# Kernel tuning notes

Hardware: AMD Instinct MI355X
Metric: run time of the kernel (lower is better)

The kernel has to match this reference:

```python
import jax, jax.numpy as jnp
import numpy as np

IN_FEATURES = 128
DEPTH = 2
UNITS = 512
BATCH = 2048
W_SCALE = 0.02


def _create_masks():
    degrees = [np.arange(IN_FEATURES)]
    for _ in range(DEPTH):
        degrees.append(np.arange(UNITS) % (IN_FEATURES - 1))
    degrees.append(degrees[0] % IN_FEATURES - 1)
    masks = []
    for d1, d2 in zip(degrees[:-1], degrees[1:]):
        masks.append(np.greater_equal(d2[:, None], d1[None, :]).astype('float32'))
    masks[-1] = np.tile(masks[-1], (2, 1))  # final layer outputs [mu; sigma]
    return masks


def setup_inputs() -> dict:
    key = jax.random.key(0)
    ks = jax.random.split(key, 7)
    m1, m2, m3 = _create_masks()
    u = jax.random.normal(ks[0], (BATCH, IN_FEATURES), dtype=jnp.float32)
    # torch.nn.Linear weight layout: [out_features, in_features]
    W1 = jax.random.normal(ks[1], (UNITS, IN_FEATURES), dtype=jnp.float32) * W_SCALE
    b1 = jax.random.normal(ks[2], (UNITS,), dtype=jnp.float32) * W_SCALE
    W2 = jax.random.normal(ks[3], (UNITS, UNITS), dtype=jnp.float32) * W_SCALE
    b2 = jax.random.normal(ks[4], (UNITS,), dtype=jnp.float32) * W_SCALE
    W3 = jax.random.normal(ks[5], (2 * IN_FEATURES, UNITS), dtype=jnp.float32) * W_SCALE
    b3 = jax.random.normal(ks[6], (2 * IN_FEATURES,), dtype=jnp.float32) * W_SCALE
    return {
        'u': u,
        'W1': W1, 'b1': b1, 'W2': W2, 'b2': b2, 'W3': W3, 'b3': b3,
        'mask1': jnp.asarray(m1), 'mask2': jnp.asarray(m2), 'mask3': jnp.asarray(m3),
    }


def reference(u, W1, b1, W2, b2, W3, b3, mask1, mask2, mask3):
    # Pre-apply masks once; math identical to masking inside every step.
    mW1 = mask1 * W1
    mW2 = mask2 * W2
    mW3 = mask3 * W3

    def conditioner(x):
        h = jax.nn.relu(x @ mW1.T + b1)
        h = jax.nn.relu(h @ mW2.T + b2)
        z = h @ mW3.T + b3  # [B, 2*IN_FEATURES]
        return z[:, :IN_FEATURES], z[:, IN_FEATURES:]  # mu, sigma

    def step(x, i):
        mu, sigma = conditioner(x)
        mu_i = jnp.take(mu, i, axis=1)        # [B]
        sig_i = jnp.take(sigma, i, axis=1)    # [B]
        u_i = jnp.take(u, i, axis=1)          # [B]
        x = x.at[:, i].set(u_i * jnp.exp(sig_i) + mu_i)
        return x, sig_i

    x0 = jnp.zeros_like(u)
    x, sigs = jax.lax.scan(step, x0, jnp.arange(IN_FEATURES))
    # sigs: [IN_FEATURES, B]; log_det_jacobian = sum_i sigma_i -> [B, 1]
    log_det_jacobian = jnp.sum(sigs, axis=0)[:, None]
    return x, log_det_jacobian
```

## Files before the change

kernel.cpp:

```cpp
#include <hip/hip_runtime.h>
#include <math.h>

static constexpr int BATCH = 2048;
static constexpr int P1_OFF = 0;
static constexpr int P2_OFF = 128 * 512;
static constexpr int P3_OFF = 128 * 512 + 512 * 512;


__device__ __forceinline__ float fc(float4 v, int k) {
    return k == 0 ? v.x : k == 1 ? v.y : k == 2 ? v.z : v.w;
}
__device__ __forceinline__ float rl(float v, int l) {
    return __int_as_float(__builtin_amdgcn_readlane(__float_as_int(v), l));
}

__global__ __launch_bounds__(256) void maf_prep(
    const float* __restrict__ W1, const float* __restrict__ W2,
    const float* __restrict__ W3, float* __restrict__ ws)
{
    float* P1 = ws + P1_OFF;
    float* P2 = ws + P2_OFF;
    float* P3 = ws + P3_OFF;
    const int NQ1 = 512 * 128 / 4;
    const int NQ2 = 512 * 512 / 4;
    const int NQ3 = 256 * 512 / 4;
    for (int q = blockIdx.x * blockDim.x + threadIdx.x; q < NQ1 + NQ2 + NQ3;
         q += gridDim.x * blockDim.x) {
        if (q < NQ1) {
            int j = q >> 5, i0 = (q & 31) * 4;
            float4 v = *(const float4*)(W1 + j * 128 + i0);
            int dj = j % 127;
            int sj = (j < 508) ? 4 * dj + (j / 127) : j;
#pragma unroll
            for (int c = 0; c < 4; ++c) {
                int i = i0 + c;
                P1[i * 512 + sj] = (dj >= i) ? fc(v, c) : 0.f;
            }
        } else if (q < NQ1 + NQ2) {
            int e = q - NQ1;
            int k = e >> 7, j0 = (e & 127) * 4;
            float4 v = *(const float4*)(W2 + k * 512 + j0);
            int dk = k % 127;
            int sk = (k < 508) ? 4 * dk + (k / 127) : k;
#pragma unroll
            for (int c = 0; c < 4; ++c) {
                int j = j0 + c;
                int dj = j % 127;
                int sj = (j < 508) ? 4 * dj + (j / 127) : j;
                P2[sj * 512 + sk] = (dk >= dj) ? fc(v, c) : 0.f;
            }
        } else {
            int e = q - NQ1 - NQ2;
            int o = e >> 7, k0 = (e & 127) * 4;
            float4 v = *(const float4*)(W3 + o * 512 + k0);
            int dd = (o & 127) - 1;
#pragma unroll
            for (int c = 0; c < 4; ++c) {
                int k = k0 + c;
                int dk = k % 127;
                int sk = (k < 508) ? 4 * dk + (k / 127) : k;
                P3[sk * 256 + o] = (dd >= dk) ? fc(v, c) : 0.f;
            }
        }
    }
}

#define DECL_WSET(P) \
    float4 P##0{}, P##1{}, P##2{}, P##3{}, P##4{}, P##5{}, P##6{}, P##7{}, \
           P##8{}, P##9{}, P##10{}, P##11{}, P##12{}, P##13{};

#define LOADS(P, LO) do { \
    if (LO) { \
        P##0 = *(const float4*)(q1); \
        P##2 = *(const float4*)(q2a); \
        P##4 = *(const float4*)(q2a + 512); \
        P##6 = *(const float4*)(q2b); \
        P##8 = *(const float4*)(q2b + 512); \
    } \
    P##1  = *(const float4*)(q1 + 256); \
    P##3  = *(const float4*)(q2a + 256); \
    P##5  = *(const float4*)(q2a + 768); \
    P##7  = *(const float4*)(q2b + 256); \
    P##9  = *(const float4*)(q2b + 768); \
    P##10 = *(const float4*)(q3); \
    P##11 = *(const float4*)(q3 + 256); \
    P##12 = *(const float4*)(q3 + 512); \
    P##13 = *(const float4*)(q3 + 768); \
    q1 += 512; q2a += 2048; q2b += 2048; q3 += 1024; \
    __builtin_amdgcn_sched_barrier(0); \
} while (0)

#define L2T(T, WLO, WHI, LO) do { \
    const float hA = rl(fmaxf(LO ? h1A[T] : h1A[4 + (T)], 0.f), l0); \
    const float hB = rl(fmaxf(LO ? h1B[T] : h1B[4 + (T)], 0.f), l0); \
    if (LO) { \
        _Pragma("unroll") for (int r = 0; r < 4; ++r) { \
            h2A[r] = fmaf(fc(WLO, r), hA, h2A[r]); \
            h2B[r] = fmaf(fc(WLO, r), hB, h2B[r]); } \
    } \
    _Pragma("unroll") for (int r = 0; r < 4; ++r) { \
        h2A[4 + r] = fmaf(fc(WHI, r), hA, h2A[4 + r]); \
        h2B[4 + r] = fmaf(fc(WHI, r), hB, h2B[4 + r]); } \
} while (0)

#define L3T(T, W4, LO) do { \
    const float gA = rl(fmaxf(LO ? h2A[T] : h2A[4 + (T)], 0.f), l0); \
    const float gB = rl(fmaxf(LO ? h2B[T] : h2B[4 + (T)], 0.f), l0); \
    _Pragma("unroll") for (int s = 0; s < 4; ++s) { \
        zA[s] = fmaf(fc(W4, s), gA, zA[s]); \
        zB[s] = fmaf(fc(W4, s), gB, zB[s]); } \
} while (0)

#define STEP(I, P, LO) do { \
    const int l0 = (I) & 63, lm = (I) >> 2, rs = (I) & 3; \
    float zsA = rs == 0 ? zA[0] : rs == 1 ? zA[1] : rs == 2 ? zA[2] : zA[3]; \
    float zsB = rs == 0 ? zB[0] : rs == 1 ? zB[1] : rs == 2 ? zB[2] : zB[3]; \
    const float muA = rl(zsA, lm), sgA = rl(zsA, 32 + lm); \
    const float muB = rl(zsB, lm), sgB = rl(zsB, 32 + lm); \
    const float uiA = rl(LO ? uA0 : uA1, l0); \
    const float uiB = rl(LO ? uB0 : uB1, l0); \
    const float xiA = fmaf(uiA, __expf(sgA), muA); \
    const float xiB = fmaf(uiB, __expf(sgB), muB); \
    ldA += sgA; ldB += sgB; \
    if (lane == l0) { \
        if (LO) { xA0 = xiA; xB0 = xiB; } else { xA1 = xiA; xB1 = xiB; } \
    } \
    if (LO) { \
        _Pragma("unroll") for (int r = 0; r < 4; ++r) { \
            h1A[r] = fmaf(fc(P##0, r), xiA, h1A[r]); \
            h1B[r] = fmaf(fc(P##0, r), xiB, h1B[r]); } \
    } \
    _Pragma("unroll") for (int r = 0; r < 4; ++r) { \
        h1A[4 + r] = fmaf(fc(P##1, r), xiA, h1A[4 + r]); \
        h1B[4 + r] = fmaf(fc(P##1, r), xiB, h1B[4 + r]); } \
    L2T(0, P##2, P##3, LO); \
    L2T(1, P##4, P##5, LO); \
    L2T(2, P##6, P##7, LO); \
    L2T(3, P##8, P##9, LO); \
    if (LO && (I) < 4) { \
        float eA = (I) == 0 ? h1A[4] : (I) == 1 ? h1A[5] : (I) == 2 ? h1A[6] : h1A[7]; \
        float eB = (I) == 0 ? h1B[4] : (I) == 1 ? h1B[5] : (I) == 2 ? h1B[6] : h1B[7]; \
        const float hA = rl(fmaxf(eA, 0.f), 63); \
        const float hB = rl(fmaxf(eB, 0.f), 63); \
        const float* wr = P2 + (508 + (I)) * 512 + 4 * lane; \
        const float4 wl = *(const float4*)(wr); \
        const float4 wh = *(const float4*)(wr + 256); \
        _Pragma("unroll") for (int r = 0; r < 4; ++r) { \
            h2A[r] = fmaf(fc(wl, r), hA, h2A[r]); \
            h2B[r] = fmaf(fc(wl, r), hB, h2B[r]); \
            h2A[4 + r] = fmaf(fc(wh, r), hA, h2A[4 + r]); \
            h2B[4 + r] = fmaf(fc(wh, r), hB, h2B[4 + r]); } \
    } \
    L3T(0, P##10, LO); \
    L3T(1, P##11, LO); \
    L3T(2, P##12, LO); \
    L3T(3, P##13, LO); \
    if (LO && (I) < 4) { \
        float eA = (I) == 0 ? h2A[4] : (I) == 1 ? h2A[5] : (I) == 2 ? h2A[6] : h2A[7]; \
        float eB = (I) == 0 ? h2B[4] : (I) == 1 ? h2B[5] : (I) == 2 ? h2B[6] : h2B[7]; \
        const float gA = rl(fmaxf(eA, 0.f), 63); \
        const float gB = rl(fmaxf(eB, 0.f), 63); \
        const float4 w4 = *(const float4*)(P3 + (508 + (I)) * 256 + 4 * lane); \
        _Pragma("unroll") for (int s = 0; s < 4; ++s) { \
            zA[s] = fmaf(fc(w4, s), gA, zA[s]); \
            zB[s] = fmaf(fc(w4, s), gB, zB[s]); } \
    } \
} while (0)

__global__ __launch_bounds__(256, 1) void maf_inverse(
    const float* __restrict__ u, const float* __restrict__ b1,
    const float* __restrict__ b2, const float* __restrict__ b3,
    const float* __restrict__ ws, float* __restrict__ out)
{
    const float* P1 = ws + P1_OFF;
    const float* P2 = ws + P2_OFF;
    const float* P3 = ws + P3_OFF;

    const int td = threadIdx.x;
    const int lane = td & 63;
    const int wid = td >> 6;
    const int rA = blockIdx.x * 8 + wid * 2;
    const int rB = rA + 1;

    float h1A[8], h1B[8], h2A[8], h2B[8];
#pragma unroll
    for (int r = 0; r < 8; ++r) {
        int s = (r < 4) ? (4 * lane + r) : (256 + 4 * lane + (r - 4));
        int i = s >> 2, t = s & 3;
        int uu = (i == 127) ? (508 + t) : (127 * t + i);
        float v1 = b1[uu], v2 = b2[uu];
        h1A[r] = v1; h1B[r] = v1; h2A[r] = v2; h2B[r] = v2;
    }
    float zA[4], zB[4];
    {
        const float4 bz = *(const float4*)(b3 + 4 * lane);
        zA[0] = bz.x; zA[1] = bz.y; zA[2] = bz.z; zA[3] = bz.w;
        zB[0] = bz.x; zB[1] = bz.y; zB[2] = bz.z; zB[3] = bz.w;
    }
    const float uA0 = u[rA * 128 + lane], uA1 = u[rA * 128 + 64 + lane];
    const float uB0 = u[rB * 128 + lane], uB1 = u[rB * 128 + 64 + lane];

    float xA0 = 0.f, xA1 = 0.f, xB0 = 0.f, xB1 = 0.f, ldA = 0.f, ldB = 0.f;

    const float* q1  = P1 + 4 * lane;
    const float* q2a = P2 + 4 * lane;
    const float* q2b = P2 + 1024 + 4 * lane;
    const float* q3  = P3 + 4 * lane;

    DECL_WSET(wa)
    DECL_WSET(wb)

    LOADS(wa, true);
#pragma unroll 1
    for (int i = 0; i < 62; i += 2) {
        LOADS(wb, true);
        STEP(i, wa, true);
        LOADS(wa, true);
        STEP(i + 1, wb, true);
    }
    LOADS(wb, true);
    STEP(62, wa, true);
    LOADS(wa, false);
    STEP(63, wb, true);
#pragma unroll 1
    for (int i = 64; i < 126; i += 2) {
        LOADS(wb, false);
        STEP(i, wa, false);
        LOADS(wa, false);
        STEP(i + 1, wb, false);
    }
    STEP(126, wa, false);

    {
        const float muA = rl(zA[3], 31), sgA = rl(zA[3], 63);
        const float muB = rl(zB[3], 31), sgB = rl(zB[3], 63);
        const float uiA = rl(uA1, 63), uiB = rl(uB1, 63);
        const float xiA = fmaf(uiA, __expf(sgA), muA);
        const float xiB = fmaf(uiB, __expf(sgB), muB);
        ldA += sgA; ldB += sgB;
        if (lane == 63) { xA1 = xiA; xB1 = xiB; }
    }

    out[rA * 128 + lane]      = xA0;
    out[rA * 128 + 64 + lane] = xA1;
    out[rB * 128 + lane]      = xB0;
    out[rB * 128 + 64 + lane] = xB1;
    if (lane == 0) {
        out[BATCH * 128 + rA] = ldA;
        out[BATCH * 128 + rB] = ldB;
    }
}

extern "C" void kernel_launch(void* const* d_in, const int* in_sizes, int n_in,
                              void* d_out, int out_size, void* d_ws, size_t ws_size,
                              hipStream_t stream)
{
    const float* u  = (const float*)d_in[0];
    const float* W1 = (const float*)d_in[1];
    const float* b1 = (const float*)d_in[2];
    const float* W2 = (const float*)d_in[3];
    const float* b2 = (const float*)d_in[4];
    const float* W3 = (const float*)d_in[5];
    const float* b3 = (const float*)d_in[6];
    float* ws  = (float*)d_ws;
    float* out = (float*)d_out;
    (void)ws_size; (void)in_sizes; (void)n_in; (void)out_size;

    maf_prep<<<448, 256, 0, stream>>>(W1, W2, W3, ws);
    maf_inverse<<<256, 256, 0, stream>>>(u, b1, b2, b3, ws, out);
}
```

Baseline: 139.1 us.

## Transpose weights through LDS in prep and skip loads of masked-zero weight rows

The prep kernel now transposes and permutes each weight matrix through padded shared-memory tiles, so global reads and float4 writes are coalesced. It replaces the old scattered scalar stores and runs on 80 blocks instead of 448. In the main inverse kernel, each step's weight loads are predicated per lane on the autoregressive degree, so lanes whose weights are known zero skip the global loads and keep the zero-initialised registers. This reduces memory traffic but adds lane divergence and relies on the register sets being zero-initialised and never refilled.

```diff
diff --git a/kernel.cpp b/kernel.cpp
--- a/kernel.cpp
+++ b/kernel.cpp
@@ -6,6 +6,16 @@
 static constexpr int P2_OFF = 128 * 512;
 static constexpr int P3_OFF = 128 * 512 + 512 * 512;
 
+__device__ __forceinline__ int sigmaF(int x) {
+    return (x < 508) ? 4 * (x % 127) + (x / 127) : x;
+}
+__device__ __forceinline__ int sigmaInv(int s) {
+    int i = s >> 2, t = s & 3;
+    return (i == 127) ? (508 + t) : (127 * t + i);
+}
+__device__ __forceinline__ int degU(int x) {
+    return (x < 508) ? (x % 127) : (x - 508);
+}
 
 __device__ __forceinline__ float fc(float4 v, int k) {
     return k == 0 ? v.x : k == 1 ? v.y : k == 2 ? v.z : v.w;
@@ -18,49 +28,80 @@
     const float* __restrict__ W1, const float* __restrict__ W2,
     const float* __restrict__ W3, float* __restrict__ ws)
 {
-    float* P1 = ws + P1_OFF;
-    float* P2 = ws + P2_OFF;
-    float* P3 = ws + P3_OFF;
-    const int NQ1 = 512 * 128 / 4;
-    const int NQ2 = 512 * 512 / 4;
-    const int NQ3 = 256 * 512 / 4;
-    for (int q = blockIdx.x * blockDim.x + threadIdx.x; q < NQ1 + NQ2 + NQ3;
-         q += gridDim.x * blockDim.x) {
-        if (q < NQ1) {
-            int j = q >> 5, i0 = (q & 31) * 4;
-            float4 v = *(const float4*)(W1 + j * 128 + i0);
-            int dj = j % 127;
-            int sj = (j < 508) ? 4 * dj + (j / 127) : j;
-#pragma unroll
-            for (int c = 0; c < 4; ++c) {
-                int i = i0 + c;
-                P1[i * 512 + sj] = (dj >= i) ? fc(v, c) : 0.f;
-            }
-        } else if (q < NQ1 + NQ2) {
-            int e = q - NQ1;
-            int k = e >> 7, j0 = (e & 127) * 4;
+    __shared__ float lds[16 * 513];
+    const int td = threadIdx.x;
+    const int b = blockIdx.x;
+    if (b < 32) {
+        for (int e = 0; e < 8; ++e) {
+            int g = e * 256 + td;
+            int l = g >> 7, j0 = (g & 127) * 4;
+            int k = sigmaInv(16 * b + l);
+            int dk = degU(k);
             float4 v = *(const float4*)(W2 + k * 512 + j0);
-            int dk = k % 127;
-            int sk = (k < 508) ? 4 * dk + (k / 127) : k;
 #pragma unroll
             for (int c = 0; c < 4; ++c) {
                 int j = j0 + c;
-                int dj = j % 127;
-                int sj = (j < 508) ? 4 * dj + (j / 127) : j;
-                P2[sj * 512 + sk] = (dk >= dj) ? fc(v, c) : 0.f;
+                lds[l * 513 + sigmaF(j)] = (dk >= degU(j)) ? fc(v, c) : 0.f;
             }
-        } else {
-            int e = q - NQ1 - NQ2;
-            int o = e >> 7, k0 = (e & 127) * 4;
+        }
+        __syncthreads();
+        for (int e = 0; e < 8; ++e) {
+            int g = e * 256 + td;
+            int sj = g >> 2, c4 = g & 3;
+            float4 o4;
+            o4.x = lds[(4 * c4 + 0) * 513 + sj];
+            o4.y = lds[(4 * c4 + 1) * 513 + sj];
+            o4.z = lds[(4 * c4 + 2) * 513 + sj];
+            o4.w = lds[(4 * c4 + 3) * 513 + sj];
+            *(float4*)(ws + P2_OFF + sj * 512 + 16 * b + 4 * c4) = o4;
+        }
+    } else if (b < 64) {
+        int bb = b - 32;
+        for (int e = 0; e < 4; ++e) {
+            int g = e * 256 + td;
+            int ol = g >> 7, k0 = (g & 127) * 4;
+            int o = 8 * bb + ol;
+            int dd = (o & 127) - 1;
             float4 v = *(const float4*)(W3 + o * 512 + k0);
-            int dd = (o & 127) - 1;
 #pragma unroll
             for (int c = 0; c < 4; ++c) {
                 int k = k0 + c;
-                int dk = k % 127;
-                int sk = (k < 508) ? 4 * dk + (k / 127) : k;
-                P3[sk * 256 + o] = (dd >= dk) ? fc(v, c) : 0.f;
+                lds[sigmaF(k) * 9 + ol] = (dd >= degU(k)) ? fc(v, c) : 0.f;
             }
+        }
+        __syncthreads();
+        for (int e = 0; e < 4; ++e) {
+            int g = e * 256 + td;
+            int sk = g >> 1, h = (g & 1) * 4;
+            float4 o4;
+            o4.x = lds[sk * 9 + h + 0];
+            o4.y = lds[sk * 9 + h + 1];
+            o4.z = lds[sk * 9 + h + 2];
+            o4.w = lds[sk * 9 + h + 3];
+            *(float4*)(ws + P3_OFF + sk * 256 + 8 * bb + h) = o4;
+        }
+    } else {
+        int bb = b - 64;
+        for (int e = 0; e < 4; ++e) {
+            int g = e * 256 + td;
+            int l = g >> 5, i0 = (g & 31) * 4;
+            int j = sigmaInv(32 * bb + l);
+            int dj = degU(j);
+            float4 v = *(const float4*)(W1 + j * 128 + i0);
+#pragma unroll
+            for (int c = 0; c < 4; ++c)
+                lds[l * 129 + i0 + c] = (dj >= i0 + c) ? fc(v, c) : 0.f;
+        }
+        __syncthreads();
+        for (int e = 0; e < 4; ++e) {
+            int g = e * 256 + td;
+            int i = g >> 3, c4 = g & 7;
+            float4 o4;
+            o4.x = lds[(4 * c4 + 0) * 129 + i];
+            o4.y = lds[(4 * c4 + 1) * 129 + i];
+            o4.z = lds[(4 * c4 + 2) * 129 + i];
+            o4.w = lds[(4 * c4 + 3) * 129 + i];
+            *(float4*)(ws + P1_OFF + i * 512 + 32 * bb + 4 * c4) = o4;
         }
     }
 }
@@ -69,8 +110,10 @@
     float4 P##0{}, P##1{}, P##2{}, P##3{}, P##4{}, P##5{}, P##6{}, P##7{}, \
            P##8{}, P##9{}, P##10{}, P##11{}, P##12{}, P##13{};
 
-#define LOADS(P, LO) do { \
-    if (LO) { \
+#define LOADS_LO(P, N) do { \
+    const int _c1 = (N); \
+    const int _c3 = ((N) + 1) >> 2; \
+    if (lane >= _c1) { \
         P##0 = *(const float4*)(q1); \
         P##2 = *(const float4*)(q2a); \
         P##4 = *(const float4*)(q2a + 512); \
@@ -82,10 +125,32 @@
     P##5  = *(const float4*)(q2a + 768); \
     P##7  = *(const float4*)(q2b + 256); \
     P##9  = *(const float4*)(q2b + 768); \
-    P##10 = *(const float4*)(q3); \
-    P##11 = *(const float4*)(q3 + 256); \
-    P##12 = *(const float4*)(q3 + 512); \
-    P##13 = *(const float4*)(q3 + 768); \
+    if ((lane & 31) >= _c3) { \
+        P##10 = *(const float4*)(q3); \
+        P##11 = *(const float4*)(q3 + 256); \
+        P##12 = *(const float4*)(q3 + 512); \
+        P##13 = *(const float4*)(q3 + 768); \
+    } \
+    q1 += 512; q2a += 2048; q2b += 2048; q3 += 1024; \
+    __builtin_amdgcn_sched_barrier(0); \
+} while (0)
+
+#define LOADS_HI(P, N) do { \
+    const int _c1 = (N) - 64; \
+    const int _c3 = ((N) + 1) >> 2; \
+    if (lane >= _c1) { \
+        P##1 = *(const float4*)(q1 + 256); \
+        P##3 = *(const float4*)(q2a + 256); \
+        P##5 = *(const float4*)(q2a + 768); \
+        P##7 = *(const float4*)(q2b + 256); \
+        P##9 = *(const float4*)(q2b + 768); \
+    } \
+    if ((lane & 31) >= _c3) { \
+        P##10 = *(const float4*)(q3); \
+        P##11 = *(const float4*)(q3 + 256); \
+        P##12 = *(const float4*)(q3 + 512); \
+        P##13 = *(const float4*)(q3 + 768); \
+    } \
     q1 += 512; q2a += 2048; q2b += 2048; q3 += 1024; \
     __builtin_amdgcn_sched_barrier(0); \
 } while (0)
@@ -186,8 +251,7 @@
 #pragma unroll
     for (int r = 0; r < 8; ++r) {
         int s = (r < 4) ? (4 * lane + r) : (256 + 4 * lane + (r - 4));
-        int i = s >> 2, t = s & 3;
-        int uu = (i == 127) ? (508 + t) : (127 * t + i);
+        int uu = sigmaInv(s);
         float v1 = b1[uu], v2 = b2[uu];
         h1A[r] = v1; h1B[r] = v1; h2A[r] = v2; h2B[r] = v2;
     }
@@ -210,23 +274,23 @@
     DECL_WSET(wa)
     DECL_WSET(wb)
 
-    LOADS(wa, true);
+    LOADS_LO(wa, 0);
 #pragma unroll 1
     for (int i = 0; i < 62; i += 2) {
-        LOADS(wb, true);
+        LOADS_LO(wb, i + 1);
         STEP(i, wa, true);
-        LOADS(wa, true);
+        LOADS_LO(wa, i + 2);
         STEP(i + 1, wb, true);
     }
-    LOADS(wb, true);
+    LOADS_LO(wb, 63);
     STEP(62, wa, true);
-    LOADS(wa, false);
+    LOADS_HI(wa, 64);
     STEP(63, wb, true);
 #pragma unroll 1
     for (int i = 64; i < 126; i += 2) {
-        LOADS(wb, false);
+        LOADS_HI(wb, i + 1);
         STEP(i, wa, false);
-        LOADS(wa, false);
+        LOADS_HI(wa, i + 2);
         STEP(i + 1, wb, false);
     }
     STEP(126, wa, false);
@@ -266,6 +330,6 @@
     float* out = (float*)d_out;
     (void)ws_size; (void)in_sizes; (void)n_in; (void)out_size;
 
-    maf_prep<<<448, 256, 0, stream>>>(W1, W2, W3, ws);
+    maf_prep<<<80, 256, 0, stream>>>(W1, W2, W3, ws);
     maf_inverse<<<256, 256, 0, stream>>>(u, b1, b2, b3, ws, out);
 }
```

New measurement: 152.3 us. 9.5% more time.

## Pack masked weights as fp16 in per-step interleaved layout to halve streaming bandwidth

Applied to the files above, without the earlier changes.

The prep kernel now converts the masked, permuted weights to fp16 and packs each step's slice of W1, W2 and W3 into one contiguous 7168-byte chunk, so each step loads a single interleaved block. The extra columns 508-511 stay in separate fp32 arrays. The inverse kernel loads uint4 fp16 pairs, converts them to fp32 and does fp32 FMAs, which halves the weight bytes streamed from L2/HBM on every step. The cost is fp16 rounding of the weights, which may push results past the tolerance, plus extra conversion instructions in the inner loop.

```diff
diff --git a/kernel.cpp b/kernel.cpp
--- a/kernel.cpp
+++ b/kernel.cpp
@@ -1,14 +1,31 @@
 #include <hip/hip_runtime.h>
+#include <hip/hip_fp16.h>
 #include <math.h>
 
 static constexpr int BATCH = 2048;
-static constexpr int P1_OFF = 0;
-static constexpr int P2_OFF = 128 * 512;
-static constexpr int P3_OFF = 128 * 512 + 512 * 512;
-
-
+
+static constexpr int STEP_BYTES = 7168;
+static constexpr int X2_FOFF    = 227584;
+static constexpr int X3_FOFF    = X2_FOFF + 2048;
+
+__device__ __forceinline__ int sigmaInvU(int s) {
+    int i = s >> 2, t = s & 3;
+    return (i == 127) ? (508 + t) : (127 * t + i);
+}
+__device__ __forceinline__ int degU(int x) {
+    return (x < 508) ? (x % 127) : (x - 508);
+}
 __device__ __forceinline__ float fc(float4 v, int k) {
     return k == 0 ? v.x : k == 1 ? v.y : k == 2 ? v.z : v.w;
+}
+__device__ __forceinline__ unsigned uc(uint4 v, int k) {
+    return k == 0 ? v.x : k == 1 ? v.y : k == 2 ? v.z : v.w;
+}
+__device__ __forceinline__ float hlo(unsigned u) {
+    return __half2float(__ushort_as_half((unsigned short)(u & 0xffffu)));
+}
+__device__ __forceinline__ float hhi(unsigned u) {
+    return __half2float(__ushort_as_half((unsigned short)(u >> 16)));
 }
 __device__ __forceinline__ float rl(float v, int l) {
     return __int_as_float(__builtin_amdgcn_readlane(__float_as_int(v), l));
@@ -18,97 +35,138 @@
     const float* __restrict__ W1, const float* __restrict__ W2,
     const float* __restrict__ W3, float* __restrict__ ws)
 {
-    float* P1 = ws + P1_OFF;
-    float* P2 = ws + P2_OFF;
-    float* P3 = ws + P3_OFF;
-    const int NQ1 = 512 * 128 / 4;
-    const int NQ2 = 512 * 512 / 4;
-    const int NQ3 = 256 * 512 / 4;
-    for (int q = blockIdx.x * blockDim.x + threadIdx.x; q < NQ1 + NQ2 + NQ3;
-         q += gridDim.x * blockDim.x) {
-        if (q < NQ1) {
-            int j = q >> 5, i0 = (q & 31) * 4;
-            float4 v = *(const float4*)(W1 + j * 128 + i0);
-            int dj = j % 127;
-            int sj = (j < 508) ? 4 * dj + (j / 127) : j;
+    const int NCH = 127 * 448;
+    int q = blockIdx.x * 256 + threadIdx.x;
+    if (q < NCH) {
+        int i = q / 448, rem = q % 448;
+        unsigned short h[8];
+        if (rem < 128) {
+            int L = rem >> 1, f = rem & 1;
+#pragma unroll
+            for (int e = 0; e < 8; ++e) {
+                int t = 2 * f + (e >> 2), c = e & 3;
+                int cu = 127 * c + L;
+                float v = (L >= i) ? W2[cu * 512 + 127 * t + i] : 0.f;
+                h[e] = __half_as_ushort(__float2half(v));
+            }
+        } else if (rem < 192) {
+            int L = rem - 128;
+#pragma unroll
+            for (int e = 0; e < 8; ++e) {
+                int s = (e < 4) ? (4 * L + e) : (256 + 4 * L + (e - 4));
+                int cu = sigmaInvU(s);
+                int dg = degU(cu);
+                float v = (dg >= i) ? W1[cu * 128 + i] : 0.f;
+                h[e] = __half_as_ushort(__float2half(v));
+            }
+        } else if (rem < 320) {
+            int idx = rem - 192, L = idx >> 1, f = idx & 1;
+#pragma unroll
+            for (int e = 0; e < 8; ++e) {
+                int t = 2 * f + (e >> 2), c = e & 3;
+                int cu = sigmaInvU(256 + 4 * L + c);
+                int dg = degU(cu);
+                float v = (dg >= i) ? W2[cu * 512 + 127 * t + i] : 0.f;
+                h[e] = __half_as_ushort(__float2half(v));
+            }
+        } else {
+            int idx = rem - 320, L = idx >> 1, f = idx & 1;
+#pragma unroll
+            for (int e = 0; e < 8; ++e) {
+                int t = 2 * f + (e >> 2), c = e & 3;
+                int o = 4 * L + c;
+                float v = ((o & 127) - 1 >= i) ? W3[o * 512 + 127 * t + i] : 0.f;
+                h[e] = __half_as_ushort(__float2half(v));
+            }
+        }
+        uint4 o4;
+        o4.x = (unsigned)h[0] | ((unsigned)h[1] << 16);
+        o4.y = (unsigned)h[2] | ((unsigned)h[3] << 16);
+        o4.z = (unsigned)h[4] | ((unsigned)h[5] << 16);
+        o4.w = (unsigned)h[6] | ((unsigned)h[7] << 16);
+        *(uint4*)((char*)ws + (size_t)q * 16) = o4;
+    } else if (q < NCH + 768) {
+        int e = q - NCH;
+        if (e < 512) {
+            int t = e >> 7, s0 = (e & 127) * 4;
+            float4 o4;
 #pragma unroll
             for (int c = 0; c < 4; ++c) {
-                int i = i0 + c;
-                P1[i * 512 + sj] = (dj >= i) ? fc(v, c) : 0.f;
-            }
-        } else if (q < NQ1 + NQ2) {
-            int e = q - NQ1;
-            int k = e >> 7, j0 = (e & 127) * 4;
-            float4 v = *(const float4*)(W2 + k * 512 + j0);
-            int dk = k % 127;
-            int sk = (k < 508) ? 4 * dk + (k / 127) : k;
+                int cu = sigmaInvU(s0 + c);
+                float v = (degU(cu) >= t) ? W2[cu * 512 + 508 + t] : 0.f;
+                if (c == 0) o4.x = v; else if (c == 1) o4.y = v;
+                else if (c == 2) o4.z = v; else o4.w = v;
+            }
+            *(float4*)(ws + X2_FOFF + t * 512 + s0) = o4;
+        } else {
+            int e2 = e - 512;
+            int t = e2 >> 6, o0 = (e2 & 63) * 4;
+            float4 o4;
 #pragma unroll
             for (int c = 0; c < 4; ++c) {
-                int j = j0 + c;
-                int dj = j % 127;
-                int sj = (j < 508) ? 4 * dj + (j / 127) : j;
-                P2[sj * 512 + sk] = (dk >= dj) ? fc(v, c) : 0.f;
-            }
-        } else {
-            int e = q - NQ1 - NQ2;
-            int o = e >> 7, k0 = (e & 127) * 4;
-            float4 v = *(const float4*)(W3 + o * 512 + k0);
-            int dd = (o & 127) - 1;
-#pragma unroll
-            for (int c = 0; c < 4; ++c) {
-                int k = k0 + c;
-                int dk = k % 127;
-                int sk = (k < 508) ? 4 * dk + (k / 127) : k;
-                P3[sk * 256 + o] = (dd >= dk) ? fc(v, c) : 0.f;
-            }
+                int o = o0 + c;
+                float v = ((o & 127) - 1 >= t) ? W3[o * 512 + 508 + t] : 0.f;
+                if (c == 0) o4.x = v; else if (c == 1) o4.y = v;
+                else if (c == 2) o4.z = v; else o4.w = v;
+            }
+            *(float4*)(ws + X3_FOFF + t * 256 + o0) = o4;
         }
     }
 }
 
 #define DECL_WSET(P) \
-    float4 P##0{}, P##1{}, P##2{}, P##3{}, P##4{}, P##5{}, P##6{}, P##7{}, \
-           P##8{}, P##9{}, P##10{}, P##11{}, P##12{}, P##13{};
-
-#define LOADS(P, LO) do { \
-    if (LO) { \
-        P##0 = *(const float4*)(q1); \
-        P##2 = *(const float4*)(q2a); \
-        P##4 = *(const float4*)(q2a + 512); \
-        P##6 = *(const float4*)(q2b); \
-        P##8 = *(const float4*)(q2b + 512); \
-    } \
-    P##1  = *(const float4*)(q1 + 256); \
-    P##3  = *(const float4*)(q2a + 256); \
-    P##5  = *(const float4*)(q2a + 768); \
-    P##7  = *(const float4*)(q2b + 256); \
-    P##9  = *(const float4*)(q2b + 768); \
-    P##10 = *(const float4*)(q3); \
-    P##11 = *(const float4*)(q3 + 256); \
-    P##12 = *(const float4*)(q3 + 512); \
-    P##13 = *(const float4*)(q3 + 768); \
-    q1 += 512; q2a += 2048; q2b += 2048; q3 += 1024; \
+    uint4 P##a0{}, P##a1{}, P##b0{}, P##b1{}, P##b2{}, P##b3{}, P##b4{};
+
+#define LOADS_LO(P) do { \
+    P##a0 = *(const uint4*)(pA); \
+    P##a1 = *(const uint4*)(pA + 16); \
+    P##b0 = *(const uint4*)(pB0); \
+    P##b1 = *(const uint4*)(pB12); \
+    P##b2 = *(const uint4*)(pB12 + 16); \
+    P##b3 = *(const uint4*)(pB34); \
+    P##b4 = *(const uint4*)(pB34 + 16); \
+    pA += STEP_BYTES; pB0 += STEP_BYTES; pB12 += STEP_BYTES; pB34 += STEP_BYTES; \
     __builtin_amdgcn_sched_barrier(0); \
 } while (0)
 
-#define L2T(T, WLO, WHI, LO) do { \
+#define LOADS_HI(P) do { \
+    P##b0 = *(const uint4*)(pB0); \
+    P##b1 = *(const uint4*)(pB12); \
+    P##b2 = *(const uint4*)(pB12 + 16); \
+    P##b3 = *(const uint4*)(pB34); \
+    P##b4 = *(const uint4*)(pB34 + 16); \
+    pA += STEP_BYTES; pB0 += STEP_BYTES; pB12 += STEP_BYTES; pB34 += STEP_BYTES; \
+    __builtin_amdgcn_sched_barrier(0); \
+} while (0)
+
+#define L2ONE(P, T, LO) do { \
     const float hA = rl(fmaxf(LO ? h1A[T] : h1A[4 + (T)], 0.f), l0); \
     const float hB = rl(fmaxf(LO ? h1B[T] : h1B[4 + (T)], 0.f), l0); \
     if (LO) { \
-        _Pragma("unroll") for (int r = 0; r < 4; ++r) { \
-            h2A[r] = fmaf(fc(WLO, r), hA, h2A[r]); \
-            h2B[r] = fmaf(fc(WLO, r), hB, h2B[r]); } \
-    } \
-    _Pragma("unroll") for (int r = 0; r < 4; ++r) { \
-        h2A[4 + r] = fmaf(fc(WHI, r), hA, h2A[4 + r]); \
-        h2B[4 + r] = fmaf(fc(WHI, r), hB, h2B[4 + r]); } \
-} while (0)
-
-#define L3T(T, W4, LO) do { \
+        const unsigned m0 = uc((T) < 2 ? P##a0 : P##a1, 2 * ((T) & 1)); \
+        const unsigned m1 = uc((T) < 2 ? P##a0 : P##a1, 2 * ((T) & 1) + 1); \
+        h2A[0] = fmaf(hlo(m0), hA, h2A[0]); h2A[1] = fmaf(hhi(m0), hA, h2A[1]); \
+        h2A[2] = fmaf(hlo(m1), hA, h2A[2]); h2A[3] = fmaf(hhi(m1), hA, h2A[3]); \
+        h2B[0] = fmaf(hlo(m0), hB, h2B[0]); h2B[1] = fmaf(hhi(m0), hB, h2B[1]); \
+        h2B[2] = fmaf(hlo(m1), hB, h2B[2]); h2B[3] = fmaf(hhi(m1), hB, h2B[3]); \
+    } \
+    const unsigned n0 = uc((T) < 2 ? P##b1 : P##b2, 2 * ((T) & 1)); \
+    const unsigned n1 = uc((T) < 2 ? P##b1 : P##b2, 2 * ((T) & 1) + 1); \
+    h2A[4] = fmaf(hlo(n0), hA, h2A[4]); h2A[5] = fmaf(hhi(n0), hA, h2A[5]); \
+    h2A[6] = fmaf(hlo(n1), hA, h2A[6]); h2A[7] = fmaf(hhi(n1), hA, h2A[7]); \
+    h2B[4] = fmaf(hlo(n0), hB, h2B[4]); h2B[5] = fmaf(hhi(n0), hB, h2B[5]); \
+    h2B[6] = fmaf(hlo(n1), hB, h2B[6]); h2B[7] = fmaf(hhi(n1), hB, h2B[7]); \
+} while (0)
+
+#define L3ONE(P, T, LO) do { \
     const float gA = rl(fmaxf(LO ? h2A[T] : h2A[4 + (T)], 0.f), l0); \
     const float gB = rl(fmaxf(LO ? h2B[T] : h2B[4 + (T)], 0.f), l0); \
-    _Pragma("unroll") for (int s = 0; s < 4; ++s) { \
-        zA[s] = fmaf(fc(W4, s), gA, zA[s]); \
-        zB[s] = fmaf(fc(W4, s), gB, zB[s]); } \
+    const unsigned p0 = uc((T) < 2 ? P##b3 : P##b4, 2 * ((T) & 1)); \
+    const unsigned p1 = uc((T) < 2 ? P##b3 : P##b4, 2 * ((T) & 1) + 1); \
+    zA[0] = fmaf(hlo(p0), gA, zA[0]); zA[1] = fmaf(hhi(p0), gA, zA[1]); \
+    zA[2] = fmaf(hlo(p1), gA, zA[2]); zA[3] = fmaf(hhi(p1), gA, zA[3]); \
+    zB[0] = fmaf(hlo(p0), gB, zB[0]); zB[1] = fmaf(hhi(p0), gB, zB[1]); \
+    zB[2] = fmaf(hlo(p1), gB, zB[2]); zB[3] = fmaf(hhi(p1), gB, zB[3]); \
 } while (0)
 
 #define STEP(I, P, LO) do { \
@@ -126,41 +184,44 @@
         if (LO) { xA0 = xiA; xB0 = xiB; } else { xA1 = xiA; xB1 = xiB; } \
     } \
     if (LO) { \
-        _Pragma("unroll") for (int r = 0; r < 4; ++r) { \
-            h1A[r] = fmaf(fc(P##0, r), xiA, h1A[r]); \
-            h1B[r] = fmaf(fc(P##0, r), xiB, h1B[r]); } \
-    } \
-    _Pragma("unroll") for (int r = 0; r < 4; ++r) { \
-        h1A[4 + r] = fmaf(fc(P##1, r), xiA, h1A[4 + r]); \
-        h1B[4 + r] = fmaf(fc(P##1, r), xiB, h1B[4 + r]); } \
-    L2T(0, P##2, P##3, LO); \
-    L2T(1, P##4, P##5, LO); \
-    L2T(2, P##6, P##7, LO); \
-    L2T(3, P##8, P##9, LO); \
+        h1A[0] = fmaf(hlo(P##b0.x), xiA, h1A[0]); \
+        h1A[1] = fmaf(hhi(P##b0.x), xiA, h1A[1]); \
+        h1A[2] = fmaf(hlo(P##b0.y), xiA, h1A[2]); \
+        h1A[3] = fmaf(hhi(P##b0.y), xiA, h1A[3]); \
+        h1B[0] = fmaf(hlo(P##b0.x), xiB, h1B[0]); \
+        h1B[1] = fmaf(hhi(P##b0.x), xiB, h1B[1]); \
+        h1B[2] = fmaf(hlo(P##b0.y), xiB, h1B[2]); \
+        h1B[3] = fmaf(hhi(P##b0.y), xiB, h1B[3]); \
+    } \
+    h1A[4] = fmaf(hlo(P##b0.z), xiA, h1A[4]); \
+    h1A[5] = fmaf(hhi(P##b0.z), xiA, h1A[5]); \
+    h1A[6] = fmaf(hlo(P##b0.w), xiA, h1A[6]); \
+    h1A[7] = fmaf(hhi(P##b0.w), xiA, h1A[7]); \
+    h1B[4] = fmaf(hlo(P##b0.z), xiB, h1B[4]); \
+    h1B[5] = fmaf(hhi(P##b0.z), xiB, h1B[5]); \
+    h1B[6] = fmaf(hlo(P##b0.w), xiB, h1B[6]); \
+    h1B[7] = fmaf(hhi(P##b0.w), xiB, h1B[7]); \
+    L2ONE(P, 0, LO); L2ONE(P, 1, LO); L2ONE(P, 2, LO); L2ONE(P, 3, LO); \
     if (LO && (I) < 4) { \
         float eA = (I) == 0 ? h1A[4] : (I) == 1 ? h1A[5] : (I) == 2 ? h1A[6] : h1A[7]; \
         float eB = (I) == 0 ? h1B[4] : (I) == 1 ? h1B[5] : (I) == 2 ? h1B[6] : h1B[7]; \
         const float hA = rl(fmaxf(eA, 0.f), 63); \
         const float hB = rl(fmaxf(eB, 0.f), 63); \
-        const float* wr = P2 + (508 + (I)) * 512 + 4 * lane; \
-        const float4 wl = *(const float4*)(wr); \
-        const float4 wh = *(const float4*)(wr + 256); \
+        const float4 wl = *(const float4*)(P2X + (I) * 512 + 4 * lane); \
+        const float4 wh = *(const float4*)(P2X + (I) * 512 + 256 + 4 * lane); \
         _Pragma("unroll") for (int r = 0; r < 4; ++r) { \
             h2A[r] = fmaf(fc(wl, r), hA, h2A[r]); \
             h2B[r] = fmaf(fc(wl, r), hB, h2B[r]); \
             h2A[4 + r] = fmaf(fc(wh, r), hA, h2A[4 + r]); \
             h2B[4 + r] = fmaf(fc(wh, r), hB, h2B[4 + r]); } \
     } \
-    L3T(0, P##10, LO); \
-    L3T(1, P##11, LO); \
-    L3T(2, P##12, LO); \
-    L3T(3, P##13, LO); \
+    L3ONE(P, 0, LO); L3ONE(P, 1, LO); L3ONE(P, 2, LO); L3ONE(P, 3, LO); \
     if (LO && (I) < 4) { \
         float eA = (I) == 0 ? h2A[4] : (I) == 1 ? h2A[5] : (I) == 2 ? h2A[6] : h2A[7]; \
         float eB = (I) == 0 ? h2B[4] : (I) == 1 ? h2B[5] : (I) == 2 ? h2B[6] : h2B[7]; \
         const float gA = rl(fmaxf(eA, 0.f), 63); \
         const float gB = rl(fmaxf(eB, 0.f), 63); \
-        const float4 w4 = *(const float4*)(P3 + (508 + (I)) * 256 + 4 * lane); \
+        const float4 w4 = *(const float4*)(P3X + (I) * 256 + 4 * lane); \
         _Pragma("unroll") for (int s = 0; s < 4; ++s) { \
             zA[s] = fmaf(fc(w4, s), gA, zA[s]); \
             zB[s] = fmaf(fc(w4, s), gB, zB[s]); } \
@@ -172,9 +233,8 @@
     const float* __restrict__ b2, const float* __restrict__ b3,
     const float* __restrict__ ws, float* __restrict__ out)
 {
-    const float* P1 = ws + P1_OFF;
-    const float* P2 = ws + P2_OFF;
-    const float* P3 = ws + P3_OFF;
+    const float* P2X = ws + X2_FOFF;
+    const float* P3X = ws + X3_FOFF;
 
     const int td = threadIdx.x;
     const int lane = td & 63;
@@ -186,8 +246,7 @@
 #pragma unroll
     for (int r = 0; r < 8; ++r) {
         int s = (r < 4) ? (4 * lane + r) : (256 + 4 * lane + (r - 4));
-        int i = s >> 2, t = s & 3;
-        int uu = (i == 127) ? (508 + t) : (127 * t + i);
+        int uu = sigmaInvU(s);
         float v1 = b1[uu], v2 = b2[uu];
         h1A[r] = v1; h1B[r] = v1; h2A[r] = v2; h2B[r] = v2;
     }
@@ -202,31 +261,31 @@
 
     float xA0 = 0.f, xA1 = 0.f, xB0 = 0.f, xB1 = 0.f, ldA = 0.f, ldB = 0.f;
 
-    const float* q1  = P1 + 4 * lane;
-    const float* q2a = P2 + 4 * lane;
-    const float* q2b = P2 + 1024 + 4 * lane;
-    const float* q3  = P3 + 4 * lane;
+    const char* pA   = (const char*)ws + 32 * lane;
+    const char* pB0  = (const char*)ws + 2048 + 16 * lane;
+    const char* pB12 = (const char*)ws + 3072 + 32 * lane;
+    const char* pB34 = (const char*)ws + 5120 + 32 * lane;
 
     DECL_WSET(wa)
     DECL_WSET(wb)
 
-    LOADS(wa, true);
+    LOADS_LO(wa);
 #pragma unroll 1
     for (int i = 0; i < 62; i += 2) {
-        LOADS(wb, true);
+        LOADS_LO(wb);
         STEP(i, wa, true);
-        LOADS(wa, true);
+        LOADS_LO(wa);
         STEP(i + 1, wb, true);
     }
-    LOADS(wb, true);
+    LOADS_LO(wb);
     STEP(62, wa, true);
-    LOADS(wa, false);
+    LOADS_HI(wa);
     STEP(63, wb, true);
 #pragma unroll 1
     for (int i = 64; i < 126; i += 2) {
-        LOADS(wb, false);
+        LOADS_HI(wb);
         STEP(i, wa, false);
-        LOADS(wa, false);
+        LOADS_HI(wa);
         STEP(i + 1, wb, false);
     }
     STEP(126, wa, false);
@@ -266,6 +325,6 @@
     float* out = (float*)d_out;
     (void)ws_size; (void)in_sizes; (void)n_in; (void)out_size;
 
-    maf_prep<<<448, 256, 0, stream>>>(W1, W2, W3, ws);
+    maf_prep<<<226, 256, 0, stream>>>(W1, W2, W3, ws);
     maf_inverse<<<256, 256, 0, stream>>>(u, b1, b2, b3, ws, out);
 }
```

Measured after the change: 137.2 us. About the same (-1.4%).
